# Optimization experiments

Measured on AMD Instinct MI355X. Metric: run time of the kernel, lower is better.

## Reference

```python
import jax, jax.numpy as jnp
import numpy as np

N = 100000
E = 1600000
IN_C, HID_C, OUT_C = 64, 128, 64


def sage_conv(x, edge_index, W_l, b_l, W_r):
    # PyG SAGEConv (mean aggr): out = lin_l(mean_{j in N(i)} x_j) + lin_r(x_i)
    src, dst = edge_index[0], edge_index[1]
    n = x.shape[0]
    msg = x[src]                                        # [E, C] gather
    agg = jax.ops.segment_sum(msg, dst, num_segments=n) # [N, C] scatter-add
    deg = jax.ops.segment_sum(jnp.ones((msg.shape[0],), x.dtype), dst, num_segments=n)
    agg = agg / jnp.maximum(deg, 1.0)[:, None]          # mean, deg-0 safe
    return agg @ W_l.T + b_l + x @ W_r.T


def setup_inputs() -> dict:
    key = jax.random.key(0)
    ks = jax.random.split(key, 8)
    x = jax.random.normal(ks[0], (N, IN_C), dtype=jnp.float32)
    edge_index = jax.random.randint(ks[1], (2, E), 0, N)
    s1 = 1.0 / np.sqrt(IN_C)
    s2 = 1.0 / np.sqrt(HID_C)
    W1_l = jax.random.uniform(ks[2], (HID_C, IN_C), jnp.float32, -s1, s1)
    W1_r = jax.random.uniform(ks[3], (HID_C, IN_C), jnp.float32, -s1, s1)
    b1 = jax.random.uniform(ks[4], (HID_C,), jnp.float32, -s1, s1)
    W2_l = jax.random.uniform(ks[5], (OUT_C, HID_C), jnp.float32, -s2, s2)
    W2_r = jax.random.uniform(ks[6], (OUT_C, HID_C), jnp.float32, -s2, s2)
    b2 = jax.random.uniform(ks[7], (OUT_C,), jnp.float32, -s2, s2)
    return {"x": x, "edge_index": edge_index, "W1_l": W1_l, "W1_r": W1_r,
            "b1": b1, "W2_l": W2_l, "W2_r": W2_r, "b2": b2}


def reference(x, edge_index, W1_l, W1_r, b1, W2_l, W2_r, b2):
    h = sage_conv(x, edge_index, W1_l, b1, W1_r)
    h = jax.nn.relu(h)
    h = sage_conv(h, edge_index, W2_l, b2, W2_r)
    return jax.nn.sigmoid(h)
```

## Files before the change

kernel.cpp:

```cpp
#include <hip/hip_runtime.h>
#include <math.h>

#define IN_C 64
#define HID_C 128
#define OUT_C 64
#define NBK 256
#define BD 64
#define GS 16

typedef __attribute__((ext_vector_type(8))) short bf16x8;
typedef __attribute__((ext_vector_type(4))) float f32x4;

__device__ __forceinline__ unsigned short f2bf(float f) {
  unsigned u = __float_as_uint(f);
  u = (u + 0x7FFFu + ((u >> 16) & 1u)) >> 16;
  return (unsigned short)u;
}
__device__ __forceinline__ float bf2f(unsigned v) {
  return __uint_as_float(v << 16);
}
__device__ __forceinline__ unsigned pack2(float a, float b) {
  return (unsigned)f2bf(a) | ((unsigned)f2bf(b) << 16);
}

__global__ __launch_bounds__(256) void k_xb(const int* __restrict__ dst,
                                            int* __restrict__ bh,
                                            const float4* __restrict__ x4,
                                            uint2* __restrict__ xh2,
                                            int E, int Mreal, int Mtot) {
  __shared__ int hh[NBK];
  int t = threadIdx.x;
  if (blockIdx.x < 1024) {
    hh[t] = 0;
    __syncthreads();
    for (int e = blockIdx.x * 256 + t; e < E; e += 1024 * 256)
      atomicAdd(&hh[dst[e] >> 9], 1);
    __syncthreads();
    if (hh[t]) atomicAdd(&bh[t * GS], hh[t]);
  } else {
    int b = blockIdx.x - 1024;
    for (int i = b * 256 + t; i < Mtot; i += 2048 * 256) {
      uint2 p = {0u, 0u};
      if (i < Mreal) {
        float4 v = x4[i];
        p.x = pack2(v.x, v.y);
        p.y = pack2(v.z, v.w);
      }
      xh2[i] = p;
    }
  }
}

__global__ __launch_bounds__(256) void k_bscan(const int* __restrict__ bh,
                                               int* __restrict__ bstart,
                                               int* __restrict__ rstart,
                                               int* __restrict__ gcur) {
  __shared__ int s1[NBK], s2[NBK];
  int t = threadIdx.x;
  int cnt = bh[t * GS];
  int region = 16 * min(cnt, (cnt >> 4) + 512);
  int creg = cnt;
  s1[t] = region; s2[t] = creg;
  __syncthreads();
  for (int off = 1; off < NBK; off <<= 1) {
    int a1 = (t >= off) ? s1[t - off] : 0;
    int a2 = (t >= off) ? s2[t - off] : 0;
    __syncthreads();
    s1[t] += a1; s2[t] += a2;
    __syncthreads();
  }
  int ex1 = s1[t] - region;
  int ex2 = s2[t] - creg;
  bstart[t] = ex1; gcur[t * GS] = ex1; rstart[t] = ex2;
}

__global__ __launch_bounds__(256) void k_msplit(const int* __restrict__ src,
                                                const int* __restrict__ dst,
                                                int* __restrict__ gcur,
                                                int* __restrict__ ebuf, int E) {
  __shared__ int bcnt[NBK], bhead[NBK];
  __shared__ int bins[BD][NBK];
  int t = threadIdx.x;
  bcnt[t] = 0; bhead[t] = 0;
  int per = (E + gridDim.x - 1) / gridDim.x;
  int e0 = blockIdx.x * per, e1 = min(E, e0 + per);
  int e = e0 + t;
  int pb[8], pv[8]; int pc = 0;
  __syncthreads();
  for (;;) {
    while (pc < 8 && e < e1) {
      int d = dst[e], s = src[e];
      pb[pc] = d >> 9; pv[pc] = (s << 9) | (d & 511);
      pc++; e += 256;
    }
    for (int q = pc - 1; q >= 0; --q) {
      int pos = atomicAdd(&bcnt[pb[q]], 1);
      if (pos < BD) {
        bins[(bhead[pb[q]] + pos) & (BD - 1)][pb[q]] = pv[q];
        pc--;
        if (q != pc) { pb[q] = pb[pc]; pv[q] = pv[pc]; }
      }
    }
    int pending = __syncthreads_count(pc > 0 || e < e1);
    int cntv = min(bcnt[t], BD);
    int head = bhead[t];
    while (cntv >= 16) {
      int base = atomicAdd(&gcur[t * GS], 16);
      int4 o[4];
#pragma unroll
      for (int k = 0; k < 16; ++k)
        ((int*)o)[k] = bins[(head + k) & (BD - 1)][t];
      int4* g = (int4*)(ebuf + base);
      g[0] = o[0]; g[1] = o[1]; g[2] = o[2]; g[3] = o[3];
      head = (head + 16) & (BD - 1);
      cntv -= 16;
    }
    bhead[t] = head;
    bcnt[t] = cntv;
    __syncthreads();
    if (!pending) break;
  }
  int cntv = bcnt[t];
  if (cntv > 0) {
    int head = bhead[t];
    int base = atomicAdd(&gcur[t * GS], 16);
#pragma unroll
    for (int k = 0; k < 16; ++k)
      ebuf[base + k] = (k < cntv) ? bins[(head + k) & (BD - 1)][t] : -1;
  }
}

__global__ __launch_bounds__(512) void k_localcsr(const int* __restrict__ ebuf,
                                                  const int* __restrict__ bstart,
                                                  const int* __restrict__ gcur,
                                                  const int* __restrict__ rstart,
                                                  int* __restrict__ csr,
                                                  int* __restrict__ row_start,
                                                  int* __restrict__ rend,
                                                  float* __restrict__ invd, int N) {
  __shared__ int lcnt[512], loff[512], lcur[512];
  int t = threadIdx.x, b = blockIdx.x;
  int start = bstart[b], endp = gcur[b * GS], rs = rstart[b];
  lcnt[t] = 0;
  __syncthreads();
  for (int i = start + t; i < endp; i += 512) {
    int pe = ebuf[i];
    if (pe != -1) atomicAdd(&lcnt[pe & 511], 1);
  }
  __syncthreads();
  int v = lcnt[t];
  loff[t] = v;
  __syncthreads();
  for (int off = 1; off < 512; off <<= 1) {
    int a = (t >= off) ? loff[t - off] : 0;
    __syncthreads();
    loff[t] += a;
    __syncthreads();
  }
  int ex = loff[t] - v;
  lcur[t] = ex;
  int node = (b << 9) + t;
  if (node < N) {
    row_start[node] = rs + ex;
    rend[node] = rs + ex + v;
    invd[node] = 1.0f / fmaxf((float)v, 1.0f);
  }
  __syncthreads();
  for (int i = start + t; i < endp; i += 512) {
    int pe = ebuf[i];
    if (pe != -1) {
      int pos = atomicAdd(&lcur[pe & 511], 1);
      csr[rs + pos] = pe >> 9;
    }
  }
}

__global__ __launch_bounds__(256) void k_gather1(const uint4* __restrict__ xh4,
                                                 const int* __restrict__ csr,
                                                 const int* __restrict__ row_start,
                                                 const int* __restrict__ rend,
                                                 const float* __restrict__ invd,
                                                 uint4* __restrict__ aggh4, int N) {
  int node = (blockIdx.x * 256 + threadIdx.x) >> 3;
  if (node >= N) return;
  int c = threadIdx.x & 7;
  int lb = threadIdx.x & 56;
  int j = row_start[node], end = rend[node];
  float a0 = 0, a1 = 0, a2 = 0, a3 = 0, a4 = 0, a5 = 0, a6 = 0, a7 = 0;
  while (__any(j < end)) {
    int q = j + c;
    q = (q < end) ? q : end - 1;
    q = (q > 0) ? q : 0;
    int sv = csr[q];
#pragma unroll
    for (int k = 0; k < 8; ++k) {
      int s = __shfl(sv, lb + k);
      if (j + k < end) {
        uint4 v = xh4[s * 8 + c];
        a0 += bf2f(v.x & 0xffffu); a1 += bf2f(v.x >> 16);
        a2 += bf2f(v.y & 0xffffu); a3 += bf2f(v.y >> 16);
        a4 += bf2f(v.z & 0xffffu); a5 += bf2f(v.z >> 16);
        a6 += bf2f(v.w & 0xffffu); a7 += bf2f(v.w >> 16);
      }
    }
    j += 8;
  }
  float inv = invd[node];
  uint4 p;
  p.x = pack2(a0 * inv, a1 * inv);
  p.y = pack2(a2 * inv, a3 * inv);
  p.z = pack2(a4 * inv, a5 * inv);
  p.w = pack2(a6 * inv, a7 * inv);
  aggh4[node * 8 + c] = p;
}

__global__ __launch_bounds__(256, 3) void k_lin1(
    const unsigned short* __restrict__ aggh, const unsigned short* __restrict__ xh,
    const float* __restrict__ W1l, const float* __restrict__ W1r,
    const float* __restrict__ b1, unsigned short* __restrict__ h, int N) {
  __shared__ __align__(16) unsigned short sW[128 * 136];
  __shared__ __align__(16) unsigned short sA[64 * 136];
  __shared__ float sb[128];
  int t = threadIdx.x;
  for (int i = t; i < 128 * 128; i += 256) {
    int o = i >> 7, k = i & 127;
    float w = (k < 64) ? W1l[o * 64 + k] : W1r[o * 64 + (k - 64)];
    sW[o * 136 + k] = f2bf(w);
  }
  if (t < 128) sb[t] = b1[t];
  int lane = t & 63, qm = lane >> 4, ln = lane & 15;
  int m0 = (t >> 6) * 16;
  __syncthreads();

  int ntiles = (N + 63) >> 6;
  for (int tile = blockIdx.x; tile < ntiles; tile += gridDim.x) {
    int base = tile << 6;
    for (int u = t; u < 64 * 64; u += 256) {
      int n = u >> 6, uu = u & 63;
      int node = base + n;
      unsigned v = 0;
      if (node < N) v = (uu < 32) ? ((const unsigned*)aggh)[node * 32 + uu]
                                  : ((const unsigned*)xh)[node * 32 + (uu - 32)];
      ((unsigned*)(sA + n * 136))[uu] = v;
    }
    __syncthreads();
    bf16x8 af[4];
#pragma unroll
    for (int kc = 0; kc < 4; ++kc)
      af[kc] = *(const bf16x8*)(sA + (m0 + ln) * 136 + kc * 32 + qm * 8);
#pragma unroll
    for (int ot = 0; ot < 8; ++ot) {
      int o0 = ot * 16;
      f32x4 acc = {0.f, 0.f, 0.f, 0.f};
#pragma unroll
      for (int kc = 0; kc < 4; ++kc) {
        bf16x8 bfr = *(const bf16x8*)(sW + (o0 + ln) * 136 + kc * 32 + qm * 8);
        acc = __builtin_amdgcn_mfma_f32_16x16x32_bf16(af[kc], bfr, acc, 0, 0, 0);
      }
      int col = o0 + ln;
      float bias = sb[col];
#pragma unroll
      for (int i = 0; i < 4; ++i) {
        int node = base + m0 + qm * 4 + i;
        if (node < N) h[node * 128 + col] = f2bf(fmaxf(acc[i] + bias, 0.f));
      }
    }
    __syncthreads();
  }
}

__global__ __launch_bounds__(256, 3) void k_lin2(
    const unsigned short* __restrict__ h, const float* __restrict__ W2l,
    const float* __restrict__ W2r, const float* __restrict__ b2,
    unsigned short* __restrict__ zh, float* __restrict__ r, int N) {
  __shared__ __align__(16) unsigned short sW[128 * 136];
  __shared__ __align__(16) unsigned short sA[64 * 136];
  __shared__ float sb2[64];
  int t = threadIdx.x;
  for (int i = t; i < 128 * 128; i += 256) {
    int u = i >> 7, k = i & 127;
    float w = (u < 64) ? W2l[u * 128 + k] : W2r[(u - 64) * 128 + k];
    sW[u * 136 + k] = f2bf(w);
  }
  if (t < 64) sb2[t] = b2[t];
  int lane = t & 63, qm = lane >> 4, ln = lane & 15;
  int m0 = (t >> 6) * 16;
  __syncthreads();

  int ntiles = (N + 63) >> 6;
  for (int tile = blockIdx.x; tile < ntiles; tile += gridDim.x) {
    int base = tile << 6;
    for (int u = t; u < 64 * 64; u += 256) {
      int n = u >> 6, uu = u & 63;
      int node = base + n;
      unsigned v = 0;
      if (node < N) v = ((const unsigned*)h)[node * 64 + uu];
      ((unsigned*)(sA + n * 136))[uu] = v;
    }
    __syncthreads();
    bf16x8 af[4];
#pragma unroll
    for (int kc = 0; kc < 4; ++kc)
      af[kc] = *(const bf16x8*)(sA + (m0 + ln) * 136 + kc * 32 + qm * 8);
#pragma unroll
    for (int ot = 0; ot < 8; ++ot) {
      int o0 = ot * 16;
      f32x4 acc = {0.f, 0.f, 0.f, 0.f};
#pragma unroll
      for (int kc = 0; kc < 4; ++kc) {
        bf16x8 bfr = *(const bf16x8*)(sW + (o0 + ln) * 136 + kc * 32 + qm * 8);
        acc = __builtin_amdgcn_mfma_f32_16x16x32_bf16(af[kc], bfr, acc, 0, 0, 0);
      }
      int u = o0 + ln;
#pragma unroll
      for (int i = 0; i < 4; ++i) {
        int node = base + m0 + qm * 4 + i;
        if (node < N) {
          if (u < 64) zh[node * 64 + u] = f2bf(acc[i]);
          else        r[node * 64 + (u - 64)] = acc[i] + sb2[u - 64];
        }
      }
    }
    __syncthreads();
  }
}

__global__ __launch_bounds__(256) void k_gather2b(const uint4* __restrict__ zh4,
                                                  const float* __restrict__ r,
                                                  const int* __restrict__ csr,
                                                  const int* __restrict__ row_start,
                                                  const int* __restrict__ rend,
                                                  const float* __restrict__ invd,
                                                  float* __restrict__ out, int N) {
  int node = (blockIdx.x * 256 + threadIdx.x) >> 3;
  if (node >= N) return;
  int c = threadIdx.x & 7;
  int lb = threadIdx.x & 56;
  int j = row_start[node], end = rend[node];
  float a0 = 0, a1 = 0, a2 = 0, a3 = 0, a4 = 0, a5 = 0, a6 = 0, a7 = 0;
  while (__any(j < end)) {
    int q = j + c;
    q = (q < end) ? q : end - 1;
    q = (q > 0) ? q : 0;
    int sv = csr[q];
#pragma unroll
    for (int k = 0; k < 8; ++k) {
      int s = __shfl(sv, lb + k);
      if (j + k < end) {
        uint4 v = zh4[s * 8 + c];
        a0 += bf2f(v.x & 0xffffu); a1 += bf2f(v.x >> 16);
        a2 += bf2f(v.y & 0xffffu); a3 += bf2f(v.y >> 16);
        a4 += bf2f(v.z & 0xffffu); a5 += bf2f(v.z >> 16);
        a6 += bf2f(v.w & 0xffffu); a7 += bf2f(v.w >> 16);
      }
    }
    j += 8;
  }
  float inv = invd[node];
  const float4* r4 = (const float4*)r;
  float4* o4 = (float4*)out;
  int bi = node * 16 + c * 2;
  float4 r0 = r4[bi], r1 = r4[bi + 1];
  float4 w0, w1;
  w0.x = 1.0f / (1.0f + __expf(-(a0 * inv + r0.x)));
  w0.y = 1.0f / (1.0f + __expf(-(a1 * inv + r0.y)));
  w0.z = 1.0f / (1.0f + __expf(-(a2 * inv + r0.z)));
  w0.w = 1.0f / (1.0f + __expf(-(a3 * inv + r0.w)));
  w1.x = 1.0f / (1.0f + __expf(-(a4 * inv + r1.x)));
  w1.y = 1.0f / (1.0f + __expf(-(a5 * inv + r1.y)));
  w1.z = 1.0f / (1.0f + __expf(-(a6 * inv + r1.z)));
  w1.w = 1.0f / (1.0f + __expf(-(a7 * inv + r1.w)));
  o4[bi] = w0;
  o4[bi + 1] = w1;
}

extern "C" void kernel_launch(void* const* d_in, const int* in_sizes, int n_in,
                              void* d_out, int out_size, void* d_ws, size_t ws_size,
                              hipStream_t stream) {
  const float* x   = (const float*)d_in[0];
  const int*   ei  = (const int*)d_in[1];
  const float* W1l = (const float*)d_in[2];
  const float* W1r = (const float*)d_in[3];
  const float* b1  = (const float*)d_in[4];
  const float* W2l = (const float*)d_in[5];
  const float* W2r = (const float*)d_in[6];
  const float* b2  = (const float*)d_in[7];
  float* out = (float*)d_out;

  int N = in_sizes[0] / IN_C;
  int E = in_sizes[1] / 2;
  const int* src = ei;
  const int* dst = ei + E;

  char* ws = (char*)d_ws;
  size_t off = 0;
  auto alignup = [](size_t v) { return (v + 511) & ~(size_t)511; };
  int* bh = (int*)(ws + off);         off = alignup(off + NBK * GS * 4);
  int* gcur = (int*)(ws + off);       off = alignup(off + NBK * GS * 4);
  int* bstart = (int*)(ws + off);     off = alignup(off + NBK * 4);
  int* rstart = (int*)(ws + off);     off = alignup(off + NBK * 4);
  int* csr = (int*)(ws + off);        off = alignup(off + ((size_t)E + NBK * 4096) * 4);
  int* row_start = (int*)(ws + off);  off = alignup(off + (size_t)N * 4);
  int* rend = (int*)(ws + off);       off = alignup(off + (size_t)N * 4);
  float* invd = (float*)(ws + off);   off = alignup(off + (size_t)N * 4);
  unsigned short* xh = (unsigned short*)(ws + off);   off = alignup(off + (size_t)(N + 1) * 64 * 2);
  unsigned short* aggh = (unsigned short*)(ws + off); off = alignup(off + (size_t)N * 64 * 2);
  unsigned short* zh = (unsigned short*)(ws + off);   off = alignup(off + (size_t)(N + 1) * 64 * 2);
  float* rbuf = (float*)(ws + off);   off = alignup(off + (size_t)N * 64 * 4);
  unsigned short* hbuf = (unsigned short*)(ws + off);
  int* ebuf = (int*)aggh;

  hipMemsetAsync(bh, 0, NBK * GS * 4, stream);
  k_xb<<<3072, 256, 0, stream>>>(dst, bh, (const float4*)x, (uint2*)xh,
                                 E, N * 16, N * 16);
  k_bscan<<<1, NBK, 0, stream>>>(bh, bstart, rstart, gcur);
  k_msplit<<<512, 256, 0, stream>>>(src, dst, gcur, ebuf, E);
  k_localcsr<<<NBK, 512, 0, stream>>>(ebuf, bstart, gcur, rstart, csr,
                                      row_start, rend, invd, N);

  k_gather1<<<(N + 31) / 32, 256, 0, stream>>>((const uint4*)xh, csr, row_start,
                                               rend, invd, (uint4*)aggh, N);
  k_lin1<<<768, 256, 0, stream>>>(aggh, xh, W1l, W1r, b1, hbuf, N);
  k_lin2<<<768, 256, 0, stream>>>(hbuf, W2l, W2r, b2, zh, rbuf, N);
  k_gather2b<<<(N + 31) / 32, 256, 0, stream>>>((const uint4*)zh, rbuf, csr,
                                                row_start, rend, invd, out, N);
}
```

Baseline: 292.6 us.

## Fuse both SAGE linear layers into one kernel and pad CSR rows to eight

The two MFMA linear kernels are merged so each 128-node tile computes the hidden activations in LDS and feeds them straight into the second layer's GEMM, removing the global write and read of the bf16 hidden buffer and one launch. MFMA operand order is swapped so outputs can be written transposed into LDS and stored as packed vectors. Separately, CSR rows are padded to multiples of eight with a dummy zero node N, so the gather loops lose per-edge bounds checks and the clamped index loads. This costs more CSR memory and some wasted gathers of the zero row, plus a 512-thread block with large LDS use and lower occupancy.

```diff
diff --git a/kernel.cpp b/kernel.cpp
--- a/kernel.cpp
+++ b/kernel.cpp
@@ -59,7 +59,7 @@
   int t = threadIdx.x;
   int cnt = bh[t * GS];
   int region = 16 * min(cnt, (cnt >> 4) + 512);
-  int creg = cnt;
+  int creg = cnt + 4096;
   s1[t] = region; s2[t] = creg;
   __syncthreads();
   for (int off = 1; off < NBK; off <<= 1) {
@@ -149,7 +149,8 @@
   }
   __syncthreads();
   int v = lcnt[t];
-  loff[t] = v;
+  int pvn = (v + 7) & ~7;
+  loff[t] = pvn;
   __syncthreads();
   for (int off = 1; off < 512; off <<= 1) {
     int a = (t >= off) ? loff[t - off] : 0;
@@ -157,12 +158,12 @@
     loff[t] += a;
     __syncthreads();
   }
-  int ex = loff[t] - v;
+  int ex = loff[t] - pvn;
   lcur[t] = ex;
   int node = (b << 9) + t;
   if (node < N) {
     row_start[node] = rs + ex;
-    rend[node] = rs + ex + v;
+    rend[node] = rs + ex + pvn;
     invd[node] = 1.0f / fmaxf((float)v, 1.0f);
   }
   __syncthreads();
@@ -173,6 +174,7 @@
       csr[rs + pos] = pe >> 9;
     }
   }
+  for (int k = ex + v; k < ex + pvn; ++k) csr[rs + k] = N;
 }
 
 __global__ __launch_bounds__(256) void k_gather1(const uint4* __restrict__ xh4,
@@ -187,23 +189,17 @@
   int lb = threadIdx.x & 56;
   int j = row_start[node], end = rend[node];
   float a0 = 0, a1 = 0, a2 = 0, a3 = 0, a4 = 0, a5 = 0, a6 = 0, a7 = 0;
-  while (__any(j < end)) {
-    int q = j + c;
-    q = (q < end) ? q : end - 1;
-    q = (q > 0) ? q : 0;
-    int sv = csr[q];
+  for (; j < end; j += 8) {
+    int sv = csr[j + c];
 #pragma unroll
     for (int k = 0; k < 8; ++k) {
       int s = __shfl(sv, lb + k);
-      if (j + k < end) {
-        uint4 v = xh4[s * 8 + c];
-        a0 += bf2f(v.x & 0xffffu); a1 += bf2f(v.x >> 16);
-        a2 += bf2f(v.y & 0xffffu); a3 += bf2f(v.y >> 16);
-        a4 += bf2f(v.z & 0xffffu); a5 += bf2f(v.z >> 16);
-        a6 += bf2f(v.w & 0xffffu); a7 += bf2f(v.w >> 16);
-      }
-    }
-    j += 8;
+      uint4 v = xh4[s * 8 + c];
+      a0 += bf2f(v.x & 0xffffu); a1 += bf2f(v.x >> 16);
+      a2 += bf2f(v.y & 0xffffu); a3 += bf2f(v.y >> 16);
+      a4 += bf2f(v.z & 0xffffu); a5 += bf2f(v.z >> 16);
+      a6 += bf2f(v.w & 0xffffu); a7 += bf2f(v.w >> 16);
+    }
   }
   float inv = invd[node];
   uint4 p;
@@ -214,110 +210,95 @@
   aggh4[node * 8 + c] = p;
 }
 
-__global__ __launch_bounds__(256, 3) void k_lin1(
+__global__ __launch_bounds__(512, 1) void k_lin12(
     const unsigned short* __restrict__ aggh, const unsigned short* __restrict__ xh,
     const float* __restrict__ W1l, const float* __restrict__ W1r,
-    const float* __restrict__ b1, unsigned short* __restrict__ h, int N) {
-  __shared__ __align__(16) unsigned short sW[128 * 136];
-  __shared__ __align__(16) unsigned short sA[64 * 136];
+    const float* __restrict__ b1, const float* __restrict__ W2l,
+    const float* __restrict__ W2r, const float* __restrict__ b2,
+    unsigned short* __restrict__ zh, float* __restrict__ r, int N) {
+  __shared__ __align__(16) unsigned short sW1[128 * 136];
+  __shared__ __align__(16) unsigned short sW2[128 * 136];
+  __shared__ __align__(16) unsigned short sAH[128 * 136];
   __shared__ float sb[128];
+  __shared__ float sb2[64];
   int t = threadIdx.x;
-  for (int i = t; i < 128 * 128; i += 256) {
+  if (blockIdx.x == 0 && t < 32) ((unsigned*)zh)[N * 32 + t] = 0;
+  for (int i = t; i < 128 * 128; i += 512) {
     int o = i >> 7, k = i & 127;
-    float w = (k < 64) ? W1l[o * 64 + k] : W1r[o * 64 + (k - 64)];
-    sW[o * 136 + k] = f2bf(w);
+    float w1 = (k < 64) ? W1l[o * 64 + k] : W1r[o * 64 + (k - 64)];
+    sW1[o * 136 + k] = f2bf(w1);
+    float w2 = (o < 64) ? W2l[o * 128 + k] : W2r[(o - 64) * 128 + k];
+    sW2[o * 136 + k] = f2bf(w2);
   }
   if (t < 128) sb[t] = b1[t];
+  else if (t < 192) sb2[t - 128] = b2[t - 128];
   int lane = t & 63, qm = lane >> 4, ln = lane & 15;
   int m0 = (t >> 6) * 16;
   __syncthreads();
 
-  int ntiles = (N + 63) >> 6;
+  int ntiles = (N + 127) >> 7;
   for (int tile = blockIdx.x; tile < ntiles; tile += gridDim.x) {
-    int base = tile << 6;
-    for (int u = t; u < 64 * 64; u += 256) {
-      int n = u >> 6, uu = u & 63;
+    int base = tile << 7;
+    for (int i = t; i < 128 * 64; i += 512) {
+      int n = i >> 6, uu = i & 63;
       int node = base + n;
       unsigned v = 0;
       if (node < N) v = (uu < 32) ? ((const unsigned*)aggh)[node * 32 + uu]
                                   : ((const unsigned*)xh)[node * 32 + (uu - 32)];
-      ((unsigned*)(sA + n * 136))[uu] = v;
+      ((unsigned*)(sAH + n * 136))[uu] = v;
     }
     __syncthreads();
     bf16x8 af[4];
 #pragma unroll
     for (int kc = 0; kc < 4; ++kc)
-      af[kc] = *(const bf16x8*)(sA + (m0 + ln) * 136 + kc * 32 + qm * 8);
+      af[kc] = *(const bf16x8*)(sAH + (m0 + ln) * 136 + kc * 32 + qm * 8);
 #pragma unroll
     for (int ot = 0; ot < 8; ++ot) {
       int o0 = ot * 16;
       f32x4 acc = {0.f, 0.f, 0.f, 0.f};
 #pragma unroll
       for (int kc = 0; kc < 4; ++kc) {
-        bf16x8 bfr = *(const bf16x8*)(sW + (o0 + ln) * 136 + kc * 32 + qm * 8);
-        acc = __builtin_amdgcn_mfma_f32_16x16x32_bf16(af[kc], bfr, acc, 0, 0, 0);
+        bf16x8 wfr = *(const bf16x8*)(sW1 + (o0 + ln) * 136 + kc * 32 + qm * 8);
+        acc = __builtin_amdgcn_mfma_f32_16x16x32_bf16(wfr, af[kc], acc, 0, 0, 0);
       }
-      int col = o0 + ln;
-      float bias = sb[col];
-#pragma unroll
-      for (int i = 0; i < 4; ++i) {
-        int node = base + m0 + qm * 4 + i;
-        if (node < N) h[node * 128 + col] = f2bf(fmaxf(acc[i] + bias, 0.f));
-      }
-    }
-    __syncthreads();
-  }
-}
-
-__global__ __launch_bounds__(256, 3) void k_lin2(
-    const unsigned short* __restrict__ h, const float* __restrict__ W2l,
-    const float* __restrict__ W2r, const float* __restrict__ b2,
-    unsigned short* __restrict__ zh, float* __restrict__ r, int N) {
-  __shared__ __align__(16) unsigned short sW[128 * 136];
-  __shared__ __align__(16) unsigned short sA[64 * 136];
-  __shared__ float sb2[64];
-  int t = threadIdx.x;
-  for (int i = t; i < 128 * 128; i += 256) {
-    int u = i >> 7, k = i & 127;
-    float w = (u < 64) ? W2l[u * 128 + k] : W2r[(u - 64) * 128 + k];
-    sW[u * 136 + k] = f2bf(w);
-  }
-  if (t < 64) sb2[t] = b2[t];
-  int lane = t & 63, qm = lane >> 4, ln = lane & 15;
-  int m0 = (t >> 6) * 16;
-  __syncthreads();
-
-  int ntiles = (N + 63) >> 6;
-  for (int tile = blockIdx.x; tile < ntiles; tile += gridDim.x) {
-    int base = tile << 6;
-    for (int u = t; u < 64 * 64; u += 256) {
-      int n = u >> 6, uu = u & 63;
-      int node = base + n;
-      unsigned v = 0;
-      if (node < N) v = ((const unsigned*)h)[node * 64 + uu];
-      ((unsigned*)(sA + n * 136))[uu] = v;
-    }
-    __syncthreads();
-    bf16x8 af[4];
+      int ob = o0 + qm * 4;
+      float h0 = fmaxf(acc[0] + sb[ob + 0], 0.f);
+      float h1 = fmaxf(acc[1] + sb[ob + 1], 0.f);
+      float h2 = fmaxf(acc[2] + sb[ob + 2], 0.f);
+      float h3 = fmaxf(acc[3] + sb[ob + 3], 0.f);
+      unsigned* hd = (unsigned*)(sAH + (m0 + ln) * 136 + ob);
+      hd[0] = pack2(h0, h1);
+      hd[1] = pack2(h2, h3);
+    }
+    bf16x8 af2[4];
 #pragma unroll
     for (int kc = 0; kc < 4; ++kc)
-      af[kc] = *(const bf16x8*)(sA + (m0 + ln) * 136 + kc * 32 + qm * 8);
+      af2[kc] = *(const bf16x8*)(sAH + (m0 + ln) * 136 + kc * 32 + qm * 8);
 #pragma unroll
     for (int ot = 0; ot < 8; ++ot) {
       int o0 = ot * 16;
       f32x4 acc = {0.f, 0.f, 0.f, 0.f};
 #pragma unroll
       for (int kc = 0; kc < 4; ++kc) {
-        bf16x8 bfr = *(const bf16x8*)(sW + (o0 + ln) * 136 + kc * 32 + qm * 8);
-        acc = __builtin_amdgcn_mfma_f32_16x16x32_bf16(af[kc], bfr, acc, 0, 0, 0);
+        bf16x8 wfr = *(const bf16x8*)(sW2 + (o0 + ln) * 136 + kc * 32 + qm * 8);
+        acc = __builtin_amdgcn_mfma_f32_16x16x32_bf16(wfr, af2[kc], acc, 0, 0, 0);
       }
-      int u = o0 + ln;
-#pragma unroll
-      for (int i = 0; i < 4; ++i) {
-        int node = base + m0 + qm * 4 + i;
-        if (node < N) {
-          if (u < 64) zh[node * 64 + u] = f2bf(acc[i]);
-          else        r[node * 64 + (u - 64)] = acc[i] + sb2[u - 64];
+      int node = base + m0 + ln;
+      int u = o0 + qm * 4;
+      if (node < N) {
+        if (u < 64) {
+          uint2 zv;
+          zv.x = pack2(acc[0], acc[1]);
+          zv.y = pack2(acc[2], acc[3]);
+          *(uint2*)(zh + node * 64 + u) = zv;
+        } else {
+          int ub = u - 64;
+          float4 rv;
+          rv.x = acc[0] + sb2[ub + 0];
+          rv.y = acc[1] + sb2[ub + 1];
+          rv.z = acc[2] + sb2[ub + 2];
+          rv.w = acc[3] + sb2[ub + 3];
+          *(float4*)(r + node * 64 + ub) = rv;
         }
       }
     }
@@ -338,23 +319,17 @@
   int lb = threadIdx.x & 56;
   int j = row_start[node], end = rend[node];
   float a0 = 0, a1 = 0, a2 = 0, a3 = 0, a4 = 0, a5 = 0, a6 = 0, a7 = 0;
-  while (__any(j < end)) {
-    int q = j + c;
-    q = (q < end) ? q : end - 1;
-    q = (q > 0) ? q : 0;
-    int sv = csr[q];
+  for (; j < end; j += 8) {
+    int sv = csr[j + c];
 #pragma unroll
     for (int k = 0; k < 8; ++k) {
       int s = __shfl(sv, lb + k);
-      if (j + k < end) {
-        uint4 v = zh4[s * 8 + c];
-        a0 += bf2f(v.x & 0xffffu); a1 += bf2f(v.x >> 16);
-        a2 += bf2f(v.y & 0xffffu); a3 += bf2f(v.y >> 16);
-        a4 += bf2f(v.z & 0xffffu); a5 += bf2f(v.z >> 16);
-        a6 += bf2f(v.w & 0xffffu); a7 += bf2f(v.w >> 16);
-      }
-    }
-    j += 8;
+      uint4 v = zh4[s * 8 + c];
+      a0 += bf2f(v.x & 0xffffu); a1 += bf2f(v.x >> 16);
+      a2 += bf2f(v.y & 0xffffu); a3 += bf2f(v.y >> 16);
+      a4 += bf2f(v.z & 0xffffu); a5 += bf2f(v.z >> 16);
+      a6 += bf2f(v.w & 0xffffu); a7 += bf2f(v.w >> 16);
+    }
   }
   float inv = invd[node];
   const float4* r4 = (const float4*)r;
@@ -407,12 +382,11 @@
   unsigned short* aggh = (unsigned short*)(ws + off); off = alignup(off + (size_t)N * 64 * 2);
   unsigned short* zh = (unsigned short*)(ws + off);   off = alignup(off + (size_t)(N + 1) * 64 * 2);
   float* rbuf = (float*)(ws + off);   off = alignup(off + (size_t)N * 64 * 4);
-  unsigned short* hbuf = (unsigned short*)(ws + off);
   int* ebuf = (int*)aggh;
 
   hipMemsetAsync(bh, 0, NBK * GS * 4, stream);
   k_xb<<<3072, 256, 0, stream>>>(dst, bh, (const float4*)x, (uint2*)xh,
-                                 E, N * 16, N * 16);
+                                 E, N * 16, (N + 1) * 16);
   k_bscan<<<1, NBK, 0, stream>>>(bh, bstart, rstart, gcur);
   k_msplit<<<512, 256, 0, stream>>>(src, dst, gcur, ebuf, E);
   k_localcsr<<<NBK, 512, 0, stream>>>(ebuf, bstart, gcur, rstart, csr,
@@ -420,8 +394,8 @@
 
   k_gather1<<<(N + 31) / 32, 256, 0, stream>>>((const uint4*)xh, csr, row_start,
                                                rend, invd, (uint4*)aggh, N);
-  k_lin1<<<768, 256, 0, stream>>>(aggh, xh, W1l, W1r, b1, hbuf, N);
-  k_lin2<<<768, 256, 0, stream>>>(hbuf, W2l, W2r, b2, zh, rbuf, N);
+  k_lin12<<<256, 512, 0, stream>>>(aggh, xh, W1l, W1r, b1, W2l, W2r, b2,
+                                   zh, rbuf, N);
   k_gather2b<<<(N + 31) / 32, 256, 0, stream>>>((const uint4*)zh, rbuf, csr,
                                                 row_start, rend, invd, out, N);
 }
```

Result: faster. 271.4 us (-7.2%).
